# Optimization experiments

Hardware: AMD Instinct MI355X
Metric: run time of the kernel (lower is better)

The kernel has to match this reference:

```python
import jax, jax.numpy as jnp
import numpy as np

N_NODES = 2048
D = 1024
B = 16384
E = 65536

def setup_inputs() -> dict:
    key = jax.random.key(0)
    ks = jax.random.split(key, 8)
    feat = jax.random.normal(ks[0], (B, 7, D), dtype=jnp.float32)
    data_x = jax.random.randint(ks[1], (7 * B,), 0, N_NODES, dtype=jnp.int64)
    adj_rows = jnp.sort(jax.random.randint(ks[2], (E,), 0, N_NODES, dtype=jnp.int32))
    adj_cols = jax.random.randint(ks[3], (E,), 0, N_NODES, dtype=jnp.int32)
    adj_vals = jax.random.uniform(ks[4], (E,), dtype=jnp.float32)
    # kaiming-uniform-like init for GCN weights, zero bias (as in reset_parameters)
    def kaiming(k, fan_in, fan_out):
        bound = jnp.sqrt(6.0 / fan_in)
        return jax.random.uniform(k, (fan_in, fan_out), minval=-bound, maxval=bound, dtype=jnp.float32)
    W1 = kaiming(ks[5], D, N_NODES)
    W2 = kaiming(ks[6], N_NODES, N_NODES)
    W3 = kaiming(ks[7], N_NODES, D)
    return {"feat": feat, "data_x": data_x, "adj_rows": adj_rows, "adj_cols": adj_cols,
            "adj_vals": adj_vals, "W1": W1, "b1": jnp.zeros((N_NODES,), jnp.float32),
            "W2": W2, "b2": jnp.zeros((N_NODES,), jnp.float32),
            "W3": W3, "b3": jnp.zeros((D,), jnp.float32)}

def reference(feat, data_x, adj_rows, adj_cols, adj_vals, W1, b1, W2, b2, W3, b3):
    n = b1.shape[0]  # number of nodes N
    e1 = data_x[0::7]  # [B]
    e2 = data_x[1::7]  # [B]
    # scatter-add: adjacency_matrix[e1] += feat[i,0]; adjacency_matrix[e2] += feat[i,1]
    idx = jnp.concatenate([e1, e2])                       # [2B]
    vals = jnp.concatenate([feat[:, 0, :], feat[:, 1, :]])  # [2B, D]
    node_feat = jax.ops.segment_sum(vals, idx, num_segments=n)  # [N, D]

    def spmm(x):  # sparse [N,N] @ dense [N,F]
        return jax.ops.segment_sum(adj_vals[:, None] * x[adj_cols], adj_rows, num_segments=n)

    h = jax.nn.relu(spmm(node_feat @ W1) + b1)  # [N, N]
    h = spmm(h @ W2) + b2                        # [N, N]
    logits = spmm(h @ W3) + b3                   # [N, D]

    # gather then swap: feat[:,0]=logits[e2], feat[:,1]=logits[e1]
    out = jnp.concatenate([logits[e2][:, None, :], logits[e1][:, None, :], feat[:, 2:, :]], axis=1)
    return out
```

## Files before the change

### kernel.cpp

```cpp
#include <hip/hip_runtime.h>
#include <stdint.h>

#define N_NODES 2048
#define DIM 1024
#define BATCH 16384
#define NEDGE 65536
#define CAP 96

typedef __bf16 bf16x8 __attribute__((ext_vector_type(8)));
typedef float f32x4 __attribute__((ext_vector_type(4)));
typedef unsigned short u16;
typedef unsigned int u32;

__device__ __forceinline__ float bf2f(u16 u) {
  union { u32 i; float f; } v; v.i = ((u32)u) << 16; return v.f;
}
__device__ __forceinline__ u16 f2bf(float f) {
  union { float f; u32 i; } v; v.f = f;
  u32 r = v.i + 0x7fffu + ((v.i >> 16) & 1u);
  return (u16)(r >> 16);
}

__device__ __forceinline__ void copy_feat_rows(const float* __restrict__ feat,
                                               float* __restrict__ out,
                                               int row0, int tid) {
  #pragma unroll 4
  for (int t = row0; t < row0 + 32; ++t) {
    int b = t / 5, s = t - b * 5 + 2;
    size_t o = ((size_t)b * 7 + s) * DIM + tid * 4;
    f32x4 v = __builtin_nontemporal_load((const f32x4*)(feat + o));
    __builtin_nontemporal_store(v, (f32x4*)(out + o));
  }
}

__global__ __launch_bounds__(256) void k_detect(const int* __restrict__ dx,
                                                const int* __restrict__ adj_rows,
                                                int* __restrict__ flag,
                                                int* __restrict__ counts,
                                                int* __restrict__ row_ptr) {
  int t = threadIdx.x;
  for (int j = t; j < N_NODES; j += 256) counts[j] = 0;
  if (t == 0) {
    int is64 = 1;
    for (int j = 0; j < 32; ++j)
      if (dx[2 * j + 1] != 0) { is64 = 0; break; }
    *flag = is64;
  }
  for (int r = t; r <= N_NODES; r += 256) {
    int lo = 0, hi = NEDGE;
    while (lo < hi) { int mid = (lo + hi) >> 1; if (adj_rows[mid] < r) lo = mid + 1; else hi = mid; }
    row_ptr[r] = lo;
  }
}

__global__ __launch_bounds__(256) void k_bucket(const int* __restrict__ dx,
                                                const int* __restrict__ flag,
                                                int* __restrict__ counts,
                                                int* __restrict__ bucket) {
  int i = blockIdx.x * 256 + threadIdx.x;
  if (i >= 2 * BATCH) return;
  int f = *flag;
  long p = (i < BATCH) ? 7L * i : 7L * (i - BATCH) + 1;
  int n = dx[f ? 2 * p : p] & (N_NODES - 1);
  int slot = atomicAdd(&counts[n], 1);
  if (slot < CAP) bucket[n * CAP + slot] = i;
}

__global__ __launch_bounds__(256) void k_nodesum(const float* __restrict__ feat,
                                                 const int* __restrict__ counts,
                                                 const int* __restrict__ bucket,
                                                 u16* __restrict__ A1) {
  int n = blockIdx.x;
  int tid = threadIdx.x;
  int cnt = counts[n]; if (cnt > CAP) cnt = CAP;
  float a0 = 0.f, a1 = 0.f, a2 = 0.f, a3 = 0.f;
  for (int j = 0; j < cnt; ++j) {
    int i = bucket[n * CAP + j];
    size_t rowoff = (i < BATCH) ? ((size_t)i * 7) * DIM
                                : ((size_t)(i - BATCH) * 7 + 1) * DIM;
    f32x4 v = *(const f32x4*)(feat + rowoff + tid * 4);
    a0 += v[0]; a1 += v[1]; a2 += v[2]; a3 += v[3];
  }
  ushort4 o; o.x = f2bf(a0); o.y = f2bf(a1); o.z = f2bf(a2); o.w = f2bf(a3);
  *(ushort4*)(A1 + (size_t)n * DIM + tid * 4) = o;
}

__global__ __launch_bounds__(256) void k_transpose3(const float* __restrict__ W1,
                                                    const float* __restrict__ W2,
                                                    const float* __restrict__ W3,
                                                    u16* __restrict__ Wt1,
                                                    u16* __restrict__ Wt2,
                                                    u16* __restrict__ Wt3) {
  __shared__ __align__(16) u16 t[32][33];
  int bid = blockIdx.x;
  const float* W; u16* Wt; int K, N, tb;
  if (bid < 2048)      { W = W1; Wt = Wt1; K = DIM;     N = N_NODES; tb = bid; }
  else if (bid < 6144) { W = W2; Wt = Wt2; K = N_NODES; N = N_NODES; tb = bid - 2048; }
  else                 { W = W3; Wt = Wt3; K = N_NODES; N = DIM;     tb = bid - 6144; }
  int ntx = N >> 5;
  int bx = tb % ntx;
  int by = tb / ntx;
  int tx = threadIdx.x & 31, ty = threadIdx.x >> 5;
  #pragma unroll
  for (int r = 0; r < 32; r += 8)
    t[r + ty][tx] = f2bf(W[(size_t)(by * 32 + r + ty) * N + bx * 32 + tx]);
  __syncthreads();
  #pragma unroll
  for (int r = 0; r < 32; r += 8)
    Wt[(size_t)(bx * 32 + r + ty) * K + by * 32 + tx] = t[tx][r + ty];
}

template <bool SCATTER>
__global__ __launch_bounds__(256) void k_spmm(const u16* __restrict__ X16,
                                              const int* __restrict__ row_ptr,
                                              const int* __restrict__ adj_cols,
                                              const float* __restrict__ adj_vals,
                                              const float* __restrict__ bias,
                                              u16* __restrict__ Y16,
                                              const int* __restrict__ counts,
                                              const int* __restrict__ bucket,
                                              const float* __restrict__ feat,
                                              float* __restrict__ out,
                                              int width, int ns, int crow0) {
  if ((int)blockIdx.x >= ns) {
    copy_feat_rows(feat, out, crow0 + ((int)blockIdx.x - ns) * 32, threadIdx.x);
    return;
  }
  int chunks = width >> 10;
  int ch = blockIdx.x % chunks;
  int r = blockIdx.x / chunks;
  int col = ch * 1024 + threadIdx.x * 4;
  int e0 = row_ptr[r], e1 = row_ptr[r + 1];
  float a0 = 0.f, a1 = 0.f, a2 = 0.f, a3 = 0.f;
  int e = e0;
  for (; e + 2 <= e1; e += 2) {
    int c0 = adj_cols[e] & (N_NODES - 1);
    int c1 = adj_cols[e + 1] & (N_NODES - 1);
    float v0 = adj_vals[e], v1 = adj_vals[e + 1];
    ushort4 x0 = *(const ushort4*)(X16 + (size_t)c0 * width + col);
    ushort4 x1 = *(const ushort4*)(X16 + (size_t)c1 * width + col);
    a0 += v0 * bf2f(x0.x) + v1 * bf2f(x1.x);
    a1 += v0 * bf2f(x0.y) + v1 * bf2f(x1.y);
    a2 += v0 * bf2f(x0.z) + v1 * bf2f(x1.z);
    a3 += v0 * bf2f(x0.w) + v1 * bf2f(x1.w);
  }
  if (e < e1) {
    int c = adj_cols[e] & (N_NODES - 1);
    float v = adj_vals[e];
    ushort4 x = *(const ushort4*)(X16 + (size_t)c * width + col);
    a0 += v * bf2f(x.x); a1 += v * bf2f(x.y);
    a2 += v * bf2f(x.z); a3 += v * bf2f(x.w);
  }
  if (SCATTER) {
    f32x4 bb = *(const f32x4*)(bias + col);
    f32x4 o; o[0] = a0 + bb[0]; o[1] = a1 + bb[1]; o[2] = a2 + bb[2]; o[3] = a3 + bb[3];
    int cnt = counts[r]; if (cnt > CAP) cnt = CAP;
    for (int j = 0; j < cnt; ++j) {
      int i = bucket[r * CAP + j];
      size_t p = (i < BATCH) ? ((size_t)i * 7 + 1) : ((size_t)(i - BATCH) * 7);
      __builtin_nontemporal_store(o, (f32x4*)(out + p * DIM + col));
    }
  } else {
    ushort4 o; o.x = f2bf(a0); o.y = f2bf(a1); o.z = f2bf(a2); o.w = f2bf(a3);
    *(ushort4*)(Y16 + (size_t)r * width + col) = o;
  }
}

template <int BM, int BN, bool BIAS, bool RELU>
__global__ __launch_bounds__(256) void k_gemm(const u16* __restrict__ A,
                                              const u16* __restrict__ Bt,
                                              const float* __restrict__ bias,
                                              u16* __restrict__ C16,
                                              const float* __restrict__ feat,
                                              float* __restrict__ out,
                                              int M, int N, int K,
                                              int ng, int crow0) {
  constexpr int BK = 64;
  constexpr int WM = BM / 2, WN = BN / 2;
  constexpr int MI = WM / 16, NI = WN / 16;
  constexpr int IA = BM / 32, IB = BN / 32;
  __shared__ __align__(16) u16 As[2][BM * BK];
  __shared__ __align__(16) u16 Bs[2][BN * BK];
  if ((int)blockIdx.x >= ng) {
    copy_feat_rows(feat, out, crow0 + ((int)blockIdx.x - ng) * 32, threadIdx.x);
    return;
  }
  const int ntx = N / BN;
  const int bx = blockIdx.x % ntx;
  const int by = blockIdx.x / ntx;
  const int tid = threadIdx.x;
  const int wid = tid >> 6;
  const int lane = tid & 63;
  const int wr = wid >> 1, wc = wid & 1;
  const int rowbase = by * BM, colbase = bx * BN;

  f32x4 acc[MI][NI];
  #pragma unroll
  for (int i = 0; i < MI; ++i)
    #pragma unroll
    for (int j = 0; j < NI; ++j) acc[i][j] = (f32x4){0.f, 0.f, 0.f, 0.f};

  const int srow = tid >> 3;
  const int skk = (((tid & 7) ^ (srow & 7)) << 3);

  #define STAGE(buf, kt)                                                        \
    do {                                                                        \
      _Pragma("unroll")                                                         \
      for (int i = 0; i < IA; ++i) {                                            \
        const u16* g = A + (size_t)(rowbase + i * 32 + srow) * K + (kt) + skk;  \
        __builtin_amdgcn_global_load_lds(                                       \
            (const __attribute__((address_space(1))) u32*)g,                    \
            (__attribute__((address_space(3))) u32*)(&As[buf][i * 2048 + tid * 8]), \
            16, 0, 0);                                                          \
      }                                                                         \
      _Pragma("unroll")                                                         \
      for (int i = 0; i < IB; ++i) {                                            \
        const u16* g = Bt + (size_t)(colbase + i * 32 + srow) * K + (kt) + skk; \
        __builtin_amdgcn_global_load_lds(                                       \
            (const __attribute__((address_space(1))) u32*)g,                    \
            (__attribute__((address_space(3))) u32*)(&Bs[buf][i * 2048 + tid * 8]), \
            16, 0, 0);                                                          \
      }                                                                         \
    } while (0)

  const int rrow = lane & 15;
  const int kq = (lane >> 4) * 8;
  const int rswz = (lane & 7) << 3;

  const int nk = K >> 6;
  STAGE(0, 0);
  __syncthreads();

  for (int t = 0; t < nk; ++t) {
    const u16* as = As[t & 1];
    const u16* bs = Bs[t & 1];
    if (t + 1 < nk) STAGE((t + 1) & 1, (t + 1) << 6);
    bf16x8 af[MI][2], bfr[NI][2];
    #pragma unroll
    for (int mi = 0; mi < MI; ++mi) {
      int r = wr * WM + mi * 16 + rrow;
      #pragma unroll
      for (int h = 0; h < 2; ++h)
        af[mi][h] = *(const bf16x8*)(as + r * 64 + ((h * 32 + kq) ^ rswz));
    }
    #pragma unroll
    for (int ni = 0; ni < NI; ++ni) {
      int c = wc * WN + ni * 16 + rrow;
      #pragma unroll
      for (int h = 0; h < 2; ++h)
        bfr[ni][h] = *(const bf16x8*)(bs + c * 64 + ((h * 32 + kq) ^ rswz));
    }
    #pragma unroll
    for (int h = 0; h < 2; ++h)
      #pragma unroll
      for (int mi = 0; mi < MI; ++mi)
        #pragma unroll
        for (int ni = 0; ni < NI; ++ni)
          acc[mi][ni] = __builtin_amdgcn_mfma_f32_16x16x32_bf16(af[mi][h], bfr[ni][h], acc[mi][ni], 0, 0, 0);
    __syncthreads();
  }
  #undef STAGE

  #pragma unroll
  for (int mi = 0; mi < MI; ++mi) {
    #pragma unroll
    for (int ni = 0; ni < NI; ++ni) {
      int col = colbase + wc * WN + ni * 16 + rrow;
      float bv = BIAS ? bias[col] : 0.f;
      #pragma unroll
      for (int j = 0; j < 4; ++j) {
        int row = rowbase + wr * WM + mi * 16 + (lane >> 4) * 4 + j;
        float v = acc[mi][ni][j] + bv;
        if (RELU) v = fmaxf(v, 0.f);
        C16[(size_t)row * N + col] = f2bf(v);
      }
    }
  }
}

__global__ __launch_bounds__(256) void k_copy(const float* __restrict__ feat,
                                              float* __restrict__ out, int crow0) {
  copy_feat_rows(feat, out, crow0 + blockIdx.x * 32, threadIdx.x);
}

extern "C" void kernel_launch(void* const* d_in, const int* in_sizes, int n_in,
                              void* d_out, int out_size, void* d_ws, size_t ws_size,
                              hipStream_t stream) {
  const float* feat   = (const float*)d_in[0];
  const int* data_x   = (const int*)d_in[1];
  const int* adj_rows = (const int*)d_in[2];
  const int* adj_cols = (const int*)d_in[3];
  const float* adj_vals = (const float*)d_in[4];
  const float* W1 = (const float*)d_in[5];
  const float* b1 = (const float*)d_in[6];
  const float* W2 = (const float*)d_in[7];
  const float* b2 = (const float*)d_in[8];
  const float* W3 = (const float*)d_in[9];
  const float* b3 = (const float*)d_in[10];
  float* out = (float*)d_out;

  char* ws = (char*)d_ws;
  size_t off = 0;
  auto alloc = [&](size_t bytes) {
    char* p = ws + off; off += (bytes + 511) & ~(size_t)511; return p;
  };
  int*  flag    = (int*)alloc(4);
  int*  counts  = (int*)alloc(N_NODES * 4);
  int*  bucket  = (int*)alloc((size_t)N_NODES * CAP * 4);
  int*  row_ptr = (int*)alloc((N_NODES + 1) * 4);
  u16*  A1      = (u16*)alloc((size_t)N_NODES * DIM * 2);
  u16*  S       = (u16*)alloc((size_t)N_NODES * N_NODES * 2);
  u16*  H       = (u16*)alloc((size_t)N_NODES * N_NODES * 2);
  u16*  X3      = (u16*)alloc((size_t)N_NODES * DIM * 2);
  u16*  Wt1     = (u16*)alloc((size_t)DIM * N_NODES * 2);
  u16*  Wt2     = (u16*)alloc((size_t)N_NODES * N_NODES * 2);
  u16*  Wt3     = (u16*)alloc((size_t)N_NODES * DIM * 2);

  k_detect<<<1, 256, 0, stream>>>(data_x, adj_rows, flag, counts, row_ptr);
  k_bucket<<<(2 * BATCH + 255) / 256, 256, 0, stream>>>(data_x, flag, counts, bucket);
  k_nodesum<<<N_NODES, 256, 0, stream>>>(feat, counts, bucket, A1);
  k_transpose3<<<8192, 256, 0, stream>>>(W1, W2, W3, Wt1, Wt2, Wt3);

  k_spmm<false><<<2048 + 256, 256, 0, stream>>>(A1, row_ptr, adj_cols, adj_vals, nullptr, S,
                                                nullptr, nullptr, feat, out, DIM, 2048, 49152);
  k_gemm<128, 64, true, true><<<512 + 512, 256, 0, stream>>>(S, Wt1, b1, H, feat, out,
                                                             N_NODES, N_NODES, DIM, 512, 0);
  k_spmm<false><<<4096 + 256, 256, 0, stream>>>(H, row_ptr, adj_cols, adj_vals, nullptr, S,
                                                nullptr, nullptr, feat, out, N_NODES, 4096, 57344);
  k_gemm<128, 64, true, false><<<512 + 512, 256, 0, stream>>>(S, Wt2, b2, H, feat, out,
                                                              N_NODES, N_NODES, N_NODES, 512, 16384);
  k_gemm<64, 64, false, false><<<512 + 512, 256, 0, stream>>>(H, Wt3, nullptr, X3, feat, out,
                                                              N_NODES, DIM, N_NODES, 512, 32768);
  k_spmm<true><<<2048 + 256, 256, 0, stream>>>(X3, row_ptr, adj_cols, adj_vals, b3, nullptr,
                                               counts, bucket, feat, out, DIM, 2048, 65536);

  k_copy<<<256, 256, 0, stream>>>(feat, out, 73728);
}
```

Baseline: 341.7 us.

## Replace bucket scatter with dense logits plus gather assemble, rebalance copy blocks

The final SpMM now writes dense fp32 logits instead of scattering each row into many output slots via buckets. A new per-output-row gather kernel then assembles slots 0 and 1. The feat-copy blocks are moved to the front of each fused launch and redistributed unevenly across kernels. The aim is to replace the load-imbalanced scatter, whose bucket lists vary in length and are capped, with a uniformly parallel gather. The cost is one extra kernel launch and an 8 MB logits round trip.

New measurement: 351.7 us. 1.03x slower.

```diff
diff --git a/kernel.cpp b/kernel.cpp
--- a/kernel.cpp
+++ b/kernel.cpp
@@ -110,25 +110,25 @@
     Wt[(size_t)(bx * 32 + r + ty) * K + by * 32 + tx] = t[tx][r + ty];
 }
 
-template <bool SCATTER>
+template <bool F32OUT>
 __global__ __launch_bounds__(256) void k_spmm(const u16* __restrict__ X16,
                                               const int* __restrict__ row_ptr,
                                               const int* __restrict__ adj_cols,
                                               const float* __restrict__ adj_vals,
                                               const float* __restrict__ bias,
                                               u16* __restrict__ Y16,
-                                              const int* __restrict__ counts,
-                                              const int* __restrict__ bucket,
+                                              float* __restrict__ Y32,
                                               const float* __restrict__ feat,
                                               float* __restrict__ out,
-                                              int width, int ns, int crow0) {
-  if ((int)blockIdx.x >= ns) {
-    copy_feat_rows(feat, out, crow0 + ((int)blockIdx.x - ns) * 32, threadIdx.x);
+                                              int width, int ncopy, int crow0) {
+  if ((int)blockIdx.x < ncopy) {
+    copy_feat_rows(feat, out, crow0 + (int)blockIdx.x * 32, threadIdx.x);
     return;
   }
+  int bid = (int)blockIdx.x - ncopy;
   int chunks = width >> 10;
-  int ch = blockIdx.x % chunks;
-  int r = blockIdx.x / chunks;
+  int ch = bid % chunks;
+  int r = bid / chunks;
   int col = ch * 1024 + threadIdx.x * 4;
   int e0 = row_ptr[r], e1 = row_ptr[r + 1];
   float a0 = 0.f, a1 = 0.f, a2 = 0.f, a3 = 0.f;
@@ -151,15 +151,10 @@
     a0 += v * bf2f(x.x); a1 += v * bf2f(x.y);
     a2 += v * bf2f(x.z); a3 += v * bf2f(x.w);
   }
-  if (SCATTER) {
+  if (F32OUT) {
     f32x4 bb = *(const f32x4*)(bias + col);
     f32x4 o; o[0] = a0 + bb[0]; o[1] = a1 + bb[1]; o[2] = a2 + bb[2]; o[3] = a3 + bb[3];
-    int cnt = counts[r]; if (cnt > CAP) cnt = CAP;
-    for (int j = 0; j < cnt; ++j) {
-      int i = bucket[r * CAP + j];
-      size_t p = (i < BATCH) ? ((size_t)i * 7 + 1) : ((size_t)(i - BATCH) * 7);
-      __builtin_nontemporal_store(o, (f32x4*)(out + p * DIM + col));
-    }
+    *(f32x4*)(Y32 + (size_t)r * width + col) = o;
   } else {
     ushort4 o; o.x = f2bf(a0); o.y = f2bf(a1); o.z = f2bf(a2); o.w = f2bf(a3);
     *(ushort4*)(Y16 + (size_t)r * width + col) = o;
@@ -174,20 +169,21 @@
                                               const float* __restrict__ feat,
                                               float* __restrict__ out,
                                               int M, int N, int K,
-                                              int ng, int crow0) {
+                                              int ncopy, int crow0) {
   constexpr int BK = 64;
   constexpr int WM = BM / 2, WN = BN / 2;
   constexpr int MI = WM / 16, NI = WN / 16;
   constexpr int IA = BM / 32, IB = BN / 32;
   __shared__ __align__(16) u16 As[2][BM * BK];
   __shared__ __align__(16) u16 Bs[2][BN * BK];
-  if ((int)blockIdx.x >= ng) {
-    copy_feat_rows(feat, out, crow0 + ((int)blockIdx.x - ng) * 32, threadIdx.x);
+  if ((int)blockIdx.x < ncopy) {
+    copy_feat_rows(feat, out, crow0 + (int)blockIdx.x * 32, threadIdx.x);
     return;
   }
+  const int bid = (int)blockIdx.x - ncopy;
   const int ntx = N / BN;
-  const int bx = blockIdx.x % ntx;
-  const int by = blockIdx.x / ntx;
+  const int bx = bid % ntx;
+  const int by = bid / ntx;
   const int tid = threadIdx.x;
   const int wid = tid >> 6;
   const int lane = tid & 63;
@@ -278,9 +274,17 @@
   }
 }
 
-__global__ __launch_bounds__(256) void k_copy(const float* __restrict__ feat,
-                                              float* __restrict__ out, int crow0) {
-  copy_feat_rows(feat, out, crow0 + blockIdx.x * 32, threadIdx.x);
+__global__ __launch_bounds__(256) void k_assemble2(const float* __restrict__ logits,
+                                                   const int* __restrict__ dx,
+                                                   const int* __restrict__ flag,
+                                                   float* __restrict__ out) {
+  int i = blockIdx.x;
+  int b = i >> 1, slot = i & 1;
+  int f = *flag;
+  long p = 7L * b + (slot == 0 ? 1 : 0);
+  int node = dx[f ? 2 * p : p] & (N_NODES - 1);
+  f32x4 v = *(const f32x4*)(logits + (size_t)node * DIM + threadIdx.x * 4);
+  __builtin_nontemporal_store(v, (f32x4*)(out + ((size_t)b * 7 + slot) * DIM + threadIdx.x * 4));
 }
 
 extern "C" void kernel_launch(void* const* d_in, const int* in_sizes, int n_in,
@@ -315,24 +319,25 @@
   u16*  Wt1     = (u16*)alloc((size_t)DIM * N_NODES * 2);
   u16*  Wt2     = (u16*)alloc((size_t)N_NODES * N_NODES * 2);
   u16*  Wt3     = (u16*)alloc((size_t)N_NODES * DIM * 2);
+  float* logits = (float*)alloc((size_t)N_NODES * DIM * 4);
 
   k_detect<<<1, 256, 0, stream>>>(data_x, adj_rows, flag, counts, row_ptr);
   k_bucket<<<(2 * BATCH + 255) / 256, 256, 0, stream>>>(data_x, flag, counts, bucket);
   k_nodesum<<<N_NODES, 256, 0, stream>>>(feat, counts, bucket, A1);
   k_transpose3<<<8192, 256, 0, stream>>>(W1, W2, W3, Wt1, Wt2, Wt3);
 
-  k_spmm<false><<<2048 + 256, 256, 0, stream>>>(A1, row_ptr, adj_cols, adj_vals, nullptr, S,
-                                                nullptr, nullptr, feat, out, DIM, 2048, 49152);
-  k_gemm<128, 64, true, true><<<512 + 512, 256, 0, stream>>>(S, Wt1, b1, H, feat, out,
-                                                             N_NODES, N_NODES, DIM, 512, 0);
-  k_spmm<false><<<4096 + 256, 256, 0, stream>>>(H, row_ptr, adj_cols, adj_vals, nullptr, S,
-                                                nullptr, nullptr, feat, out, N_NODES, 4096, 57344);
-  k_gemm<128, 64, true, false><<<512 + 512, 256, 0, stream>>>(S, Wt2, b2, H, feat, out,
-                                                              N_NODES, N_NODES, N_NODES, 512, 16384);
-  k_gemm<64, 64, false, false><<<512 + 512, 256, 0, stream>>>(H, Wt3, nullptr, X3, feat, out,
-                                                              N_NODES, DIM, N_NODES, 512, 32768);
-  k_spmm<true><<<2048 + 256, 256, 0, stream>>>(X3, row_ptr, adj_cols, adj_vals, b3, nullptr,
-                                               counts, bucket, feat, out, DIM, 2048, 65536);
-
-  k_copy<<<256, 256, 0, stream>>>(feat, out, 73728);
-}
+  k_spmm<false><<<256 + 2048, 256, 0, stream>>>(A1, row_ptr, adj_cols, adj_vals, nullptr, S,
+                                                nullptr, feat, out, DIM, 256, 0);
+  k_gemm<128, 64, true, true><<<384 + 512, 256, 0, stream>>>(S, Wt1, b1, H, feat, out,
+                                                             N_NODES, N_NODES, DIM, 384, 8192);
+  k_spmm<false><<<448 + 4096, 256, 0, stream>>>(H, row_ptr, adj_cols, adj_vals, nullptr, S,
+                                                nullptr, feat, out, N_NODES, 448, 20480);
+  k_gemm<128, 64, true, false><<<576 + 512, 256, 0, stream>>>(S, Wt2, b2, H, feat, out,
+                                                              N_NODES, N_NODES, N_NODES, 576, 34816);
+  k_gemm<64, 64, false, false><<<384 + 512, 256, 0, stream>>>(H, Wt3, nullptr, X3, feat, out,
+                                                              N_NODES, DIM, N_NODES, 384, 53248);
+  k_spmm<true><<<512 + 2048, 256, 0, stream>>>(X3, row_ptr, adj_cols, adj_vals, b3, nullptr,
+                                               logits, feat, out, DIM, 512, 65536);
+
+  k_assemble2<<<2 * BATCH, 256, 0, stream>>>(logits, data_x, flag, out);
+}
```
